# Optimization experiments

Measured on AMD Instinct MI355X. Metric: run time of the kernel, lower is better.

## Reference

```python
import jax, jax.numpy as jnp
import numpy as np

N, E, C_IN, C_OUT = 8192, 262144, 64, 64


def setup_inputs() -> dict:
    key = jax.random.key(0)
    k1, k2, k3 = jax.random.split(key, 3)
    x = jax.random.normal(k1, (N, C_IN), dtype=jnp.float32)
    edge_index = jax.random.randint(k2, (2, E), 0, N, dtype=jnp.int32)
    # xavier_uniform init for Linear weight [out, in], zeros bias (matches reset_parameters)
    limit = float(np.sqrt(6.0 / (C_IN + C_OUT)))
    W = jax.random.uniform(k3, (C_OUT, C_IN), dtype=jnp.float32, minval=-limit, maxval=limit)
    b = jnp.zeros((C_OUT,), dtype=jnp.float32)
    return {"x": x, "edge_index": edge_index, "W": W, "b": b}


def reference(x, edge_index, W, b):
    n = x.shape[0]
    # dense adjacency with set-semantics scatter (duplicate edges collapse to 1.0)
    adj = jnp.zeros((n, n), dtype=x.dtype).at[edge_index[0], edge_index[1]].set(1.0)
    adj = adj + jnp.eye(n, dtype=x.dtype)  # diagonal can become 2.0 on self-loop edges, as in torch
    degree = adj.sum(axis=1)               # row-sum degree (asymmetric graphs use out-degree)
    dinv = jnp.where(degree > 0, degree ** -0.5, 0.0)
    norm_adj = dinv[:, None] * adj * dinv[None, :]
    h = norm_adj @ x                        # [N, C_in]
    return h @ W.T + b                      # [N, C_out]
```

## Files before the change

### kernel.cpp

```cpp
#include <hip/hip_runtime.h>

#define N_NODES 8192
#define WPR 256
#define C 64
#define CAP 512

__global__ __launch_bounds__(256) void zero_bitmap(uint4* __restrict__ bm4) {
    int i = blockIdx.x * 256 + threadIdx.x;
    bm4[i] = make_uint4(0u, 0u, 0u, 0u);
}

__global__ __launch_bounds__(256) void scatter_edges(const int* __restrict__ e, int E,
                              unsigned* __restrict__ bitmap) {
    int i = blockIdx.x * blockDim.x + threadIdx.x;
    if (i < E) {
        int r = e[i];
        int c = e[i + E];
        atomicOr(&bitmap[r * WPR + (c >> 5)], 1u << (c & 31));
    }
}

__global__ __launch_bounds__(256) void degree_kernel(const unsigned* __restrict__ bitmap,
                               float* __restrict__ dinv) {
    int wave = threadIdx.x >> 6;
    int lane = threadIdx.x & 63;
    int r = blockIdx.x * 4 + wave;
    const uint4* row = (const uint4*)(bitmap + (size_t)r * WPR);
    uint4 v = row[lane];
    int cnt = __popc(v.x) + __popc(v.y) + __popc(v.z) + __popc(v.w);
#pragma unroll
    for (int off = 32; off; off >>= 1) cnt += __shfl_down(cnt, off);
    if (lane == 0) dinv[r] = 1.0f / sqrtf((float)(cnt + 1));
}

__global__ __launch_bounds__(256) void gemm_ys(const float* __restrict__ x,
                        const float* __restrict__ W,
                        const float* __restrict__ dinv,
                        float* __restrict__ ys) {
    __shared__ float Wt[C * C];
    int tid = threadIdx.x;
    for (int i = tid; i < C * C; i += 256) {
        int o = i >> 6, k = i & 63;
        Wt[k * C + o] = W[i];
    }
    __syncthreads();
    int o = tid & 63;
    int r = blockIdx.x * 4 + (tid >> 6);
    const float* xr = x + (size_t)r * C;
    float acc = 0.0f;
#pragma unroll
    for (int k = 0; k < C; ++k) acc += xr[k] * Wt[k * C + o];
    ys[(size_t)r * C + o] = dinv[r] * acc;
}

__global__ __launch_bounds__(256) void spmm_kernel(const unsigned* __restrict__ bitmap,
                            const float* __restrict__ dinv,
                            const float* __restrict__ ys,
                            const float* __restrict__ b,
                            float* __restrict__ out) {
    __shared__ unsigned short list[4][CAP];
    int wave = threadIdx.x >> 6;
    int lane = threadIdx.x & 63;
    int r = blockIdx.x * 4 + wave;
    const uint4* row = (const uint4*)(bitmap + (size_t)r * WPR);
    uint4 v = row[lane];
    int myc = __popc(v.x) + __popc(v.y) + __popc(v.z) + __popc(v.w);

    int pre = myc;
#pragma unroll
    for (int d = 1; d < 64; d <<= 1) {
        int t = __shfl_up(pre, d);
        if (lane >= d) pre += t;
    }
    int total = __shfl(pre, 63);
    int woff = pre - myc;
    bool uselist = (total <= CAP);

    if (uselist) {
        unsigned short* L = list[wave];
        int base = lane * 128;
        unsigned bits;
        bits = v.x;
        while (bits) { L[woff++] = (unsigned short)(base       + __builtin_ctz(bits)); bits &= bits - 1; }
        bits = v.y;
        while (bits) { L[woff++] = (unsigned short)(base + 32  + __builtin_ctz(bits)); bits &= bits - 1; }
        bits = v.z;
        while (bits) { L[woff++] = (unsigned short)(base + 64  + __builtin_ctz(bits)); bits &= bits - 1; }
        bits = v.w;
        while (bits) { L[woff++] = (unsigned short)(base + 96  + __builtin_ctz(bits)); bits &= bits - 1; }
    }
    __syncthreads();

    float acc = ys[(size_t)r * C + lane];
    if (uselist) {
        const unsigned short* L = list[wave];
        float a0 = 0.f, a1 = 0.f, a2 = 0.f, a3 = 0.f;
        int i = 0;
        for (; i + 4 <= total; i += 4) {
            int c0 = L[i], c1 = L[i + 1], c2 = L[i + 2], c3 = L[i + 3];
            a0 += ys[(size_t)c0 * C + lane];
            a1 += ys[(size_t)c1 * C + lane];
            a2 += ys[(size_t)c2 * C + lane];
            a3 += ys[(size_t)c3 * C + lane];
        }
        for (; i < total; ++i) acc += ys[(size_t)L[i] * C + lane];
        acc += (a0 + a1) + (a2 + a3);
    } else {
        for (int w4 = 0; w4 < WPR / 4; ++w4) {
            uint4 vv = row[w4];
            int base = w4 * 128;
            unsigned bits;
            bits = vv.x; while (bits) { int c = base       + __builtin_ctz(bits); bits &= bits - 1; acc += ys[(size_t)c * C + lane]; }
            bits = vv.y; while (bits) { int c = base + 32  + __builtin_ctz(bits); bits &= bits - 1; acc += ys[(size_t)c * C + lane]; }
            bits = vv.z; while (bits) { int c = base + 64  + __builtin_ctz(bits); bits &= bits - 1; acc += ys[(size_t)c * C + lane]; }
            bits = vv.w; while (bits) { int c = base + 96  + __builtin_ctz(bits); bits &= bits - 1; acc += ys[(size_t)c * C + lane]; }
        }
    }
    out[(size_t)r * C + lane] = dinv[r] * acc + b[lane];
}

extern "C" void kernel_launch(void* const* d_in, const int* in_sizes, int n_in,
                              void* d_out, int out_size, void* d_ws, size_t ws_size,
                              hipStream_t stream) {
    const float* x  = (const float*)d_in[0];
    const int*   ei = (const int*)d_in[1];
    const float* W  = (const float*)d_in[2];
    const float* b  = (const float*)d_in[3];
    float* out = (float*)d_out;
    int E = in_sizes[1] / 2;

    unsigned* bitmap = (unsigned*)d_ws;
    float* dinv = (float*)((char*)d_ws + (size_t)N_NODES * WPR * 4);
    float* ys   = dinv + N_NODES;

    zero_bitmap<<<2048, 256, 0, stream>>>((uint4*)bitmap);
    scatter_edges<<<(E + 255) / 256, 256, 0, stream>>>(ei, E, bitmap);
    degree_kernel<<<N_NODES / 4, 256, 0, stream>>>(bitmap, dinv);
    gemm_ys<<<N_NODES / 4, 256, 0, stream>>>(x, W, dinv, ys);
    spmm_kernel<<<N_NODES / 4, 256, 0, stream>>>(bitmap, dinv, ys, b, out);
}
```

Baseline: 51.56 us.

## Fuse kernels: count degrees during scatter, merge zero-init with GEMM

```diff
diff --git a/kernel.cpp b/kernel.cpp
--- a/kernel.cpp
+++ b/kernel.cpp
@@ -4,41 +4,21 @@
 #define WPR 256
 #define C 64
 #define CAP 512
+#define GEMM_BLOCKS 2048
 
-__global__ __launch_bounds__(256) void zero_bitmap(uint4* __restrict__ bm4) {
-    int i = blockIdx.x * 256 + threadIdx.x;
-    bm4[i] = make_uint4(0u, 0u, 0u, 0u);
-}
-
-__global__ __launch_bounds__(256) void scatter_edges(const int* __restrict__ e, int E,
-                              unsigned* __restrict__ bitmap) {
-    int i = blockIdx.x * blockDim.x + threadIdx.x;
-    if (i < E) {
-        int r = e[i];
-        int c = e[i + E];
-        atomicOr(&bitmap[r * WPR + (c >> 5)], 1u << (c & 31));
+__global__ __launch_bounds__(256) void init_gemm(const float* __restrict__ x,
+                          const float* __restrict__ W,
+                          float* __restrict__ y,
+                          uint4* __restrict__ bm4,
+                          int* __restrict__ deg) {
+    int tid = threadIdx.x;
+    if (blockIdx.x >= GEMM_BLOCKS) {
+        int zb = blockIdx.x - GEMM_BLOCKS;
+        bm4[zb * 256 + tid] = make_uint4(0u, 0u, 0u, 0u);
+        if (tid < 4) deg[zb * 4 + tid] = 0;
+        return;
     }
-}
-
-__global__ __launch_bounds__(256) void degree_kernel(const unsigned* __restrict__ bitmap,
-                               float* __restrict__ dinv) {
-    int wave = threadIdx.x >> 6;
-    int lane = threadIdx.x & 63;
-    int r = blockIdx.x * 4 + wave;
-    const uint4* row = (const uint4*)(bitmap + (size_t)r * WPR);
-    uint4 v = row[lane];
-    int cnt = __popc(v.x) + __popc(v.y) + __popc(v.z) + __popc(v.w);
-#pragma unroll
-    for (int off = 32; off; off >>= 1) cnt += __shfl_down(cnt, off);
-    if (lane == 0) dinv[r] = 1.0f / sqrtf((float)(cnt + 1));
-}
-
-__global__ __launch_bounds__(256) void gemm_ys(const float* __restrict__ x,
-                        const float* __restrict__ W,
-                        const float* __restrict__ dinv,
-                        float* __restrict__ ys) {
     __shared__ float Wt[C * C];
-    int tid = threadIdx.x;
     for (int i = tid; i < C * C; i += 256) {
         int o = i >> 6, k = i & 63;
         Wt[k * C + o] = W[i];
@@ -50,12 +30,34 @@
     float acc = 0.0f;
 #pragma unroll
     for (int k = 0; k < C; ++k) acc += xr[k] * Wt[k * C + o];
-    ys[(size_t)r * C + o] = dinv[r] * acc;
+    y[(size_t)r * C + o] = acc;
+}
+
+__global__ __launch_bounds__(256) void scatter_deg(const int* __restrict__ e, int E,
+                            unsigned* __restrict__ bitmap,
+                            int* __restrict__ deg) {
+    int j = blockIdx.x * 256 + threadIdx.x;
+    int i = j * 2;
+    if (i + 1 < E) {
+        int2 rr = *(const int2*)(e + i);
+        int2 cc = *(const int2*)(e + E + i);
+        unsigned bit0 = 1u << (cc.x & 31);
+        unsigned bit1 = 1u << (cc.y & 31);
+        unsigned old0 = atomicOr(&bitmap[(size_t)rr.x * WPR + (cc.x >> 5)], bit0);
+        unsigned old1 = atomicOr(&bitmap[(size_t)rr.y * WPR + (cc.y >> 5)], bit1);
+        if (!(old0 & bit0)) atomicAdd(&deg[rr.x], 1);
+        if (!(old1 & bit1)) atomicAdd(&deg[rr.y], 1);
+    } else if (i < E) {
+        int r = e[i], c = e[E + i];
+        unsigned bit = 1u << (c & 31);
+        unsigned old = atomicOr(&bitmap[(size_t)r * WPR + (c >> 5)], bit);
+        if (!(old & bit)) atomicAdd(&deg[r], 1);
+    }
 }
 
 __global__ __launch_bounds__(256) void spmm_kernel(const unsigned* __restrict__ bitmap,
-                            const float* __restrict__ dinv,
-                            const float* __restrict__ ys,
+                            const int* __restrict__ deg,
+                            const float* __restrict__ y,
                             const float* __restrict__ b,
                             float* __restrict__ out) {
     __shared__ unsigned short list[4][CAP];
@@ -75,9 +77,9 @@
     int total = __shfl(pre, 63);
     int woff = pre - myc;
     bool uselist = (total <= CAP);
+    unsigned short* L = list[wave];
 
     if (uselist) {
-        unsigned short* L = list[wave];
         int base = lane * 128;
         unsigned bits;
         bits = v.x;
@@ -89,34 +91,50 @@
         bits = v.w;
         while (bits) { L[woff++] = (unsigned short)(base + 96  + __builtin_ctz(bits)); bits &= bits - 1; }
     }
-    __syncthreads();
 
-    float acc = ys[(size_t)r * C + lane];
+    float dr = rsqrtf((float)(deg[r] + 1));
+    float acc = dr * y[(size_t)r * C + lane];
     if (uselist) {
-        const unsigned short* L = list[wave];
         float a0 = 0.f, a1 = 0.f, a2 = 0.f, a3 = 0.f;
+        float a4 = 0.f, a5 = 0.f, a6 = 0.f, a7 = 0.f;
         int i = 0;
-        for (; i + 4 <= total; i += 4) {
-            int c0 = L[i], c1 = L[i + 1], c2 = L[i + 2], c3 = L[i + 3];
-            a0 += ys[(size_t)c0 * C + lane];
-            a1 += ys[(size_t)c1 * C + lane];
-            a2 += ys[(size_t)c2 * C + lane];
-            a3 += ys[(size_t)c3 * C + lane];
+        for (; i + 8 <= total; i += 8) {
+            int c0 = L[i], c1 = L[i+1], c2 = L[i+2], c3 = L[i+3];
+            int c4 = L[i+4], c5 = L[i+5], c6 = L[i+6], c7 = L[i+7];
+            float w0 = rsqrtf((float)(deg[c0] + 1));
+            float w1 = rsqrtf((float)(deg[c1] + 1));
+            float w2 = rsqrtf((float)(deg[c2] + 1));
+            float w3 = rsqrtf((float)(deg[c3] + 1));
+            float w4 = rsqrtf((float)(deg[c4] + 1));
+            float w5 = rsqrtf((float)(deg[c5] + 1));
+            float w6 = rsqrtf((float)(deg[c6] + 1));
+            float w7 = rsqrtf((float)(deg[c7] + 1));
+            a0 += w0 * y[c0 * C + lane];
+            a1 += w1 * y[c1 * C + lane];
+            a2 += w2 * y[c2 * C + lane];
+            a3 += w3 * y[c3 * C + lane];
+            a4 += w4 * y[c4 * C + lane];
+            a5 += w5 * y[c5 * C + lane];
+            a6 += w6 * y[c6 * C + lane];
+            a7 += w7 * y[c7 * C + lane];
         }
-        for (; i < total; ++i) acc += ys[(size_t)L[i] * C + lane];
-        acc += (a0 + a1) + (a2 + a3);
+        for (; i < total; ++i) {
+            int c = L[i];
+            acc += rsqrtf((float)(deg[c] + 1)) * y[c * C + lane];
+        }
+        acc += ((a0 + a1) + (a2 + a3)) + ((a4 + a5) + (a6 + a7));
     } else {
-        for (int w4 = 0; w4 < WPR / 4; ++w4) {
-            uint4 vv = row[w4];
-            int base = w4 * 128;
+        for (int w4i = 0; w4i < WPR / 4; ++w4i) {
+            uint4 vv = row[w4i];
+            int base = w4i * 128;
             unsigned bits;
-            bits = vv.x; while (bits) { int c = base       + __builtin_ctz(bits); bits &= bits - 1; acc += ys[(size_t)c * C + lane]; }
-            bits = vv.y; while (bits) { int c = base + 32  + __builtin_ctz(bits); bits &= bits - 1; acc += ys[(size_t)c * C + lane]; }
-            bits = vv.z; while (bits) { int c = base + 64  + __builtin_ctz(bits); bits &= bits - 1; acc += ys[(size_t)c * C + lane]; }
-            bits = vv.w; while (bits) { int c = base + 96  + __builtin_ctz(bits); bits &= bits - 1; acc += ys[(size_t)c * C + lane]; }
+            bits = vv.x; while (bits) { int c = base       + __builtin_ctz(bits); bits &= bits - 1; acc += rsqrtf((float)(deg[c] + 1)) * y[c * C + lane]; }
+            bits = vv.y; while (bits) { int c = base + 32  + __builtin_ctz(bits); bits &= bits - 1; acc += rsqrtf((float)(deg[c] + 1)) * y[c * C + lane]; }
+            bits = vv.z; while (bits) { int c = base + 64  + __builtin_ctz(bits); bits &= bits - 1; acc += rsqrtf((float)(deg[c] + 1)) * y[c * C + lane]; }
+            bits = vv.w; while (bits) { int c = base + 96  + __builtin_ctz(bits); bits &= bits - 1; acc += rsqrtf((float)(deg[c] + 1)) * y[c * C + lane]; }
         }
     }
-    out[(size_t)r * C + lane] = dinv[r] * acc + b[lane];
+    out[(size_t)r * C + lane] = dr * acc + b[lane];
 }
 
 extern "C" void kernel_launch(void* const* d_in, const int* in_sizes, int n_in,
@@ -130,12 +148,10 @@
     int E = in_sizes[1] / 2;
 
     unsigned* bitmap = (unsigned*)d_ws;
-    float* dinv = (float*)((char*)d_ws + (size_t)N_NODES * WPR * 4);
-    float* ys   = dinv + N_NODES;
+    int*   deg = (int*)((char*)d_ws + (size_t)N_NODES * WPR * 4);
+    float* y   = (float*)(deg + N_NODES);
 
-    zero_bitmap<<<2048, 256, 0, stream>>>((uint4*)bitmap);
-    scatter_edges<<<(E + 255) / 256, 256, 0, stream>>>(ei, E, bitmap);
-    degree_kernel<<<N_NODES / 4, 256, 0, stream>>>(bitmap, dinv);
-    gemm_ys<<<N_NODES / 4, 256, 0, stream>>>(x, W, dinv, ys);
-    spmm_kernel<<<N_NODES / 4, 256, 0, stream>>>(bitmap, dinv, ys, b, out);
+    init_gemm<<<2 * GEMM_BLOCKS, 256, 0, stream>>>(x, W, y, (uint4*)bitmap, deg);
+    scatter_deg<<<(E / 2 + 255) / 256, 256, 0, stream>>>(ei, E, bitmap, deg);
+    spmm_kernel<<<N_NODES / 4, 256, 0, stream>>>(bitmap, deg, y, b, out);
 }
```

After: 70.99 us. +37.7%, slower.
